# Kernel tuning notes

Hardware: AMD Instinct MI355X
Metric: run time of the kernel (lower is better)

Reference implementation:

```python
import jax, jax.numpy as jnp
import numpy as np

B, T, S_ENC, D, H, E, K = 4, 1024, 64, 1024, 16, 8, 2
DK = D // H
HID = 4 * D
NEG = -65504.0
EPS = 1e-5


def rmsnorm(x, w):
    return w * (x * jax.lax.rsqrt(jnp.mean(x * x, axis=-1, keepdims=True) + EPS))


def mha(xq, xk, xv, mask, wq, wk, wv, wo):
    # linear (no bias): y = x @ W.T
    q = jnp.einsum('bsd,ed->bse', xq, wq).reshape(xq.shape[0], -1, H, DK).transpose(0, 2, 1, 3)
    k = jnp.einsum('bsd,ed->bse', xk, wk).reshape(xk.shape[0], -1, H, DK).transpose(0, 2, 1, 3)
    v = jnp.einsum('bsd,ed->bse', xv, wv).reshape(xv.shape[0], -1, H, DK).transpose(0, 2, 1, 3)
    scores = jnp.einsum('bhqd,bhkd->bhqk', q, k) / jnp.sqrt(jnp.float32(DK))
    scores = jnp.where(mask[:, None, :, :] == 0, NEG, scores)
    attn = jax.nn.softmax(scores, axis=-1)
    out = jnp.einsum('bhqk,bhkd->bhqd', attn, v)
    out = out.transpose(0, 2, 1, 3).reshape(xq.shape[0], -1, D)
    return jnp.einsum('bsd,ed->bse', out, wo)


def moe_ffn(x, gate_w, exp_w1, exp_w2, sh_w1, sh_w2):
    b, s, d = x.shape
    xf = x.reshape(-1, d)                                     # [N, D]
    # shared expert
    sh = jnp.einsum('nd,hd->nh', xf, sh_w1)
    sh = jax.nn.silu(sh)
    sh = jnp.einsum('nh,dh->nd', sh, sh_w2)
    # gating
    logits = jnp.einsum('nd,ed->ne', xf, gate_w)              # [N, E]
    topk_vals, topk_idx = jax.lax.top_k(logits, K)
    topk_gates = jax.nn.softmax(topk_vals, axis=-1)
    n = xf.shape[0]
    gates = jnp.zeros((n, E), dtype=xf.dtype).at[jnp.arange(n)[:, None], topk_idx].set(topk_gates)
    # all experts computed densely (as in the torch code), then gated
    h = jnp.einsum('nd,ehd->neh', xf, exp_w1)                 # [N, E, 4D]
    h = jax.nn.silu(h)
    eo = jnp.einsum('neh,edh->ned', h, exp_w2)                # [N, E, D]
    sel = jnp.einsum('ned,ne->nd', eo, gates)
    return (sh + sel).reshape(b, s, d)


def setup_inputs() -> dict:
    key = jax.random.key(0)
    ks = jax.random.split(key, 16)
    sd = 1.0 / np.sqrt(D)
    inp = {
        'x': jax.random.normal(ks[0], (B, T, D), jnp.float32),
        'encoder_output': jax.random.normal(ks[1], (B, S_ENC, D), jnp.float32),
        'tgt_mask': jnp.tril(jnp.ones((T, T), jnp.int32))[None].repeat(B, 0),
        'src_mask': jnp.ones((B, T, S_ENC), jnp.int32),
        'norm1_w': jnp.ones((D,), jnp.float32),
        'norm2_w': jnp.ones((D,), jnp.float32),
        'norm3_w': jnp.ones((D,), jnp.float32),
        'sa_wq': jax.random.normal(ks[2], (D, D), jnp.float32) * sd,
        'sa_wk': jax.random.normal(ks[3], (D, D), jnp.float32) * sd,
        'sa_wv': jax.random.normal(ks[4], (D, D), jnp.float32) * sd,
        'sa_wo': jax.random.normal(ks[5], (D, D), jnp.float32) * sd,
        'ca_wq': jax.random.normal(ks[6], (D, D), jnp.float32) * sd,
        'ca_wk': jax.random.normal(ks[7], (D, D), jnp.float32) * sd,
        'ca_wv': jax.random.normal(ks[8], (D, D), jnp.float32) * sd,
        'ca_wo': jax.random.normal(ks[9], (D, D), jnp.float32) * sd,
        'gate_w': jax.random.normal(ks[10], (E, D), jnp.float32) * 0.02,
        'exp_w1': jax.random.normal(ks[11], (E, HID, D), jnp.float32) * sd,
        'exp_w2': jax.random.normal(ks[12], (E, D, HID), jnp.float32) / np.sqrt(HID),
        'sh_w1': jax.random.normal(ks[13], (HID, D), jnp.float32) * sd,
        'sh_w2': jax.random.normal(ks[14], (D, HID), jnp.float32) / np.sqrt(HID),
    }
    return inp


def reference(x, encoder_output, tgt_mask, src_mask, norm1_w, norm2_w, norm3_w,
              sa_wq, sa_wk, sa_wv, sa_wo, ca_wq, ca_wk, ca_wv, ca_wo,
              gate_w, exp_w1, exp_w2, sh_w1, sh_w2):
    xn = rmsnorm(x, norm1_w)
    h = x + mha(xn, xn, xn, tgt_mask, sa_wq, sa_wk, sa_wv, sa_wo)
    hn = rmsnorm(h, norm2_w)
    h = h + mha(hn, encoder_output, encoder_output, src_mask, ca_wq, ca_wk, ca_wv, ca_wo)
    hn = rmsnorm(h, norm3_w)
    return h + moe_ffn(hn, gate_w, exp_w1, exp_w2, sh_w1, sh_w2)
```

## Files before the change

kernel.cpp:

```cpp
#include <hip/hip_runtime.h>
#include <hip/hip_bf16.h>
#include <cstdint>
#include <cstddef>
#include <math.h>

typedef __attribute__((ext_vector_type(8))) short bf16x8;
typedef __attribute__((ext_vector_type(4))) float f32x4;
typedef __attribute__((ext_vector_type(4))) short s16x4;

static __device__ __forceinline__ short f2bf(float f) {
  union { __hip_bfloat16 b; short s; } u;
  u.b = __float2bfloat16(f);
  return u.s;
}

static __device__ __forceinline__ float bf2f(short s) {
  union { unsigned u; float f; } v;
  v.u = ((unsigned)(unsigned short)s) << 16;
  return v.f;
}

static __device__ __forceinline__ void gload_lds16(const short* g, short* l) {
  __builtin_amdgcn_global_load_lds((const __attribute__((address_space(1))) void*)g,
                                   (__attribute__((address_space(3))) void*)l,
                                   16, 0, 0);
}

__global__ __launch_bounds__(256) void cvt_k(const float* __restrict__ src,
                                             short* __restrict__ dst, long n4) {
  long i = (long)blockIdx.x * blockDim.x + threadIdx.x;
  long stride = (long)gridDim.x * blockDim.x;
  for (; i < n4; i += stride) {
    float4 v = ((const float4*)src)[i];
    s16x4 o;
    o.x = f2bf(v.x); o.y = f2bf(v.y); o.z = f2bf(v.z); o.w = f2bf(v.w);
    ((s16x4*)dst)[i] = o;
  }
}

__global__ __launch_bounds__(256) void cvt2_k(const float* __restrict__ src,
                                              short* __restrict__ hi,
                                              short* __restrict__ lo, long n4) {
  long i = (long)blockIdx.x * blockDim.x + threadIdx.x;
  long stride = (long)gridDim.x * blockDim.x;
  for (; i < n4; i += stride) {
    float4 v = ((const float4*)src)[i];
    s16x4 h, l;
    h.x = f2bf(v.x); l.x = f2bf(v.x - bf2f(h.x));
    h.y = f2bf(v.y); l.y = f2bf(v.y - bf2f(h.y));
    h.z = f2bf(v.z); l.z = f2bf(v.z - bf2f(h.z));
    h.w = f2bf(v.w); l.w = f2bf(v.w - bf2f(h.w));
    ((s16x4*)hi)[i] = h;
    ((s16x4*)lo)[i] = l;
  }
}

__global__ __launch_bounds__(256) void rms2_k(const float* __restrict__ x,
                                              const float* __restrict__ w,
                                              short* __restrict__ hi,
                                              short* __restrict__ lo) {
  const int row = blockIdx.x, tid = threadIdx.x;
  const float* xr = x + (size_t)row * 1024;
  float4 v = *(const float4*)&xr[tid * 4];
  float ss = v.x * v.x + v.y * v.y + v.z * v.z + v.w * v.w;
#pragma unroll
  for (int off = 32; off; off >>= 1) ss += __shfl_down(ss, off);
  __shared__ float red[4];
  if ((tid & 63) == 0) red[tid >> 6] = ss;
  __syncthreads();
  float rs = rsqrtf((red[0] + red[1] + red[2] + red[3]) * (1.f / 1024.f) + 1e-5f);
  float4 wv = *(const float4*)&w[tid * 4];
  float o0 = v.x * rs * wv.x, o1 = v.y * rs * wv.y;
  float o2 = v.z * rs * wv.z, o3 = v.w * rs * wv.w;
  s16x4 h, l;
  h.x = f2bf(o0); l.x = f2bf(o0 - bf2f(h.x));
  h.y = f2bf(o1); l.y = f2bf(o1 - bf2f(h.y));
  h.z = f2bf(o2); l.z = f2bf(o2 - bf2f(h.z));
  h.w = f2bf(o3); l.w = f2bf(o3 - bf2f(h.w));
  const size_t ib = (size_t)row * 1024 + tid * 4;
  *(s16x4*)&hi[ib] = h;
  *(s16x4*)&lo[ib] = l;
}

__global__ __launch_bounds__(256) void rms_k(const float* __restrict__ x,
                                             const float* __restrict__ w,
                                             short* __restrict__ obf) {
  const int row = blockIdx.x, tid = threadIdx.x;
  const float* xr = x + (size_t)row * 1024;
  float4 v = *(const float4*)&xr[tid * 4];
  float ss = v.x * v.x + v.y * v.y + v.z * v.z + v.w * v.w;
#pragma unroll
  for (int off = 32; off; off >>= 1) ss += __shfl_down(ss, off);
  __shared__ float red[4];
  if ((tid & 63) == 0) red[tid >> 6] = ss;
  __syncthreads();
  float rs = rsqrtf((red[0] + red[1] + red[2] + red[3]) * (1.f / 1024.f) + 1e-5f);
  float4 wv = *(const float4*)&w[tid * 4];
  s16x4 ob;
  ob.x = f2bf(v.x * rs * wv.x); ob.y = f2bf(v.y * rs * wv.y);
  ob.z = f2bf(v.z * rs * wv.z); ob.w = f2bf(v.w * rs * wv.w);
  *(s16x4*)&obf[(size_t)row * 1024 + tid * 4] = ob;
}

template <int EPI>
__global__ __launch_bounds__(256)
void gemm3_k(const short* __restrict__ Ah, const short* __restrict__ Al,
             const short* __restrict__ Bh, const short* __restrict__ Bl,
             float* __restrict__ C, const float* __restrict__ resid,
             short* __restrict__ Ch, short* __restrict__ Cl,
             int M, int N, int K) {
  __shared__ short sAh[128 * 32];
  __shared__ short sAl[128 * 32];
  __shared__ short sBh[128 * 32];
  __shared__ short sBl[128 * 32];

  const int bn = blockIdx.x, bm = blockIdx.y;
  const int tid = threadIdx.x;
  const int lane = tid & 63, wv = tid >> 6;
  const int rch = lane >> 2;
  const int cch = (((lane & 3) ^ (rch & 3)) << 3);
  const int wr = wv >> 1, wc = wv & 1;
  const int lr = lane & 15, lg = lane >> 4;
  const int c0 = wv * 2, c1 = wv * 2 + 1;
  const int sw = ((lg ^ (lr & 3)) << 3);

  const int ra0 = bm * 128 + c0 * 16 + rch;
  const int ra1 = bm * 128 + c1 * 16 + rch;
  const int rb0 = bn * 128 + c0 * 16 + rch, rb1 = bn * 128 + c1 * 16 + rch;

  f32x4 acc[4][4];
#pragma unroll
  for (int m = 0; m < 4; m++)
#pragma unroll
    for (int n = 0; n < 4; n++) acc[m][n] = (f32x4){0.f, 0.f, 0.f, 0.f};

  const int nk = K >> 5;
  for (int kt = 0; kt < nk; ++kt) {
    __syncthreads();
    const int colk = (kt << 5) + cch;
    gload_lds16(Ah + (size_t)ra0 * K + colk, &sAh[c0 * 512]);
    gload_lds16(Ah + (size_t)ra1 * K + colk, &sAh[c1 * 512]);
    gload_lds16(Al + (size_t)ra0 * K + colk, &sAl[c0 * 512]);
    gload_lds16(Al + (size_t)ra1 * K + colk, &sAl[c1 * 512]);
    gload_lds16(Bh + (size_t)rb0 * K + colk, &sBh[c0 * 512]);
    gload_lds16(Bh + (size_t)rb1 * K + colk, &sBh[c1 * 512]);
    gload_lds16(Bl + (size_t)rb0 * K + colk, &sBl[c0 * 512]);
    gload_lds16(Bl + (size_t)rb1 * K + colk, &sBl[c1 * 512]);
    __syncthreads();
    bf16x8 ah[4], al[4], bh[4], bl[4];
#pragma unroll
    for (int m = 0; m < 4; m++) {
      const int o = (wr * 64 + m * 16 + lr) * 32 + sw;
      ah[m] = *(const bf16x8*)&sAh[o];
      al[m] = *(const bf16x8*)&sAl[o];
    }
#pragma unroll
    for (int n = 0; n < 4; n++) {
      const int o = (wc * 64 + n * 16 + lr) * 32 + sw;
      bh[n] = *(const bf16x8*)&sBh[o];
      bl[n] = *(const bf16x8*)&sBl[o];
    }
#pragma unroll
    for (int m = 0; m < 4; m++)
#pragma unroll
      for (int n = 0; n < 4; n++) {
        acc[m][n] = __builtin_amdgcn_mfma_f32_16x16x32_bf16(ah[m], bh[n], acc[m][n], 0, 0, 0);
        acc[m][n] = __builtin_amdgcn_mfma_f32_16x16x32_bf16(al[m], bh[n], acc[m][n], 0, 0, 0);
        acc[m][n] = __builtin_amdgcn_mfma_f32_16x16x32_bf16(ah[m], bl[n], acc[m][n], 0, 0, 0);
      }
  }

  const int cbase = bn * 128 + wc * 64;
#pragma unroll
  for (int m = 0; m < 4; m++) {
    const int rl = bm * 128 + wr * 64 + m * 16 + lg * 4;
#pragma unroll
    for (int n = 0; n < 4; n++) {
      f32x4 v = acc[m][n];
      const int col = cbase + n * 16 + lr;
#pragma unroll
      for (int j = 0; j < 4; j++) {
        const size_t idx = (size_t)(rl + j) * N + col;
        if (EPI == 0) {
          C[idx] = v[j];
        } else if (EPI == 2) {
          C[idx] = v[j] + resid[idx];
        } else {
          short hh = f2bf(v[j]);
          Ch[idx] = hh;
          Cl[idx] = f2bf(v[j] - bf2f(hh));
        }
      }
    }
  }
}

template <bool CAUSAL>
__global__ __launch_bounds__(256)
void attn3_k(const short* __restrict__ Qh, const short* __restrict__ Ql, int ldq,
             const short* __restrict__ Kh, const short* __restrict__ Kl, int ldk,
             const short* __restrict__ Vh, const short* __restrict__ Vl, int ldv,
             short* __restrict__ Oh, short* __restrict__ Ol, int ldo,
             int Tq, int Tkv, float scale) {
  __shared__ short sKh[64 * 72], sKl[64 * 72];
  __shared__ short sVh[64 * 72], sVl[64 * 72];
  __shared__ short sPh[4][16 * 72], sPl[4][16 * 72];

  const int idx = blockIdx.x;
  const int qb = 15 - (idx >> 6);
  const int h = (idx >> 2) & 15;
  const int b = idx & 3;
  const int tid = threadIdx.x, lane = tid & 63, wv = tid >> 6;
  const int hoff = h * 64;
  const int lr = lane & 15, lg = lane >> 4;
  const int qlo = wv * 16;

  bf16x8 qhf[2], qlf[2];
  {
    const size_t qrow = (size_t)(b * Tq + qb * 64 + qlo + lr) * ldq + hoff;
#pragma unroll
    for (int ks = 0; ks < 2; ks++) {
      qhf[ks] = *(const bf16x8*)&Qh[qrow + ks * 32 + lg * 8];
      qlf[ks] = *(const bf16x8*)&Ql[qrow + ks * 32 + lg * 8];
    }
  }

  float m_run = -1e30f, l_run = 0.f;
  f32x4 o[4];
#pragma unroll
  for (int n = 0; n < 4; n++) o[n] = (f32x4){0.f, 0.f, 0.f, 0.f};

  const int ntiles = CAUSAL ? (qb + 1) : (Tkv >> 6);
  for (int kt = 0; kt < ntiles; ++kt) {
    __syncthreads();
#pragma unroll
    for (int j = 0; j < 2; j++) {
      int c = j * 256 + tid;
      int row = c >> 3, col = (c & 7) << 3;
      size_t gk = (size_t)(b * Tkv + kt * 64 + row) * ldk + hoff + col;
      *(bf16x8*)&sKh[row * 72 + col] = *(const bf16x8*)&Kh[gk];
      *(bf16x8*)&sKl[row * 72 + col] = *(const bf16x8*)&Kl[gk];
      size_t gv = (size_t)(b * Tkv + kt * 64 + row) * ldv + hoff + col;
      bf16x8 vh = *(const bf16x8*)&Vh[gv];
      bf16x8 vl = *(const bf16x8*)&Vl[gv];
#pragma unroll
      for (int i = 0; i < 8; i++) {
        sVh[(col + i) * 72 + row] = vh[i];
        sVl[(col + i) * 72 + row] = vl[i];
      }
    }
    __syncthreads();

    f32x4 st[4];
#pragma unroll
    for (int jk = 0; jk < 4; jk++) st[jk] = (f32x4){0.f, 0.f, 0.f, 0.f};
#pragma unroll
    for (int ks = 0; ks < 2; ks++) {
#pragma unroll
      for (int jk = 0; jk < 4; jk++) {
        const int o2 = (jk * 16 + lr) * 72 + ks * 32 + lg * 8;
        bf16x8 kh = *(const bf16x8*)&sKh[o2];
        bf16x8 kl = *(const bf16x8*)&sKl[o2];
        st[jk] = __builtin_amdgcn_mfma_f32_16x16x32_bf16(kh, qhf[ks], st[jk], 0, 0, 0);
        st[jk] = __builtin_amdgcn_mfma_f32_16x16x32_bf16(kl, qhf[ks], st[jk], 0, 0, 0);
        st[jk] = __builtin_amdgcn_mfma_f32_16x16x32_bf16(kh, qlf[ks], st[jk], 0, 0, 0);
      }
    }

    const int qg = qb * 64 + qlo + lr;
    float s[16];
    float tmax = -1e30f;
#pragma unroll
    for (int jk = 0; jk < 4; jk++)
#pragma unroll
      for (int r2 = 0; r2 < 4; r2++) {
        float xv = st[jk][r2] * scale;
        if (CAUSAL && kt == qb) {
          int kvidx = kt * 64 + jk * 16 + lg * 4 + r2;
          if (kvidx > qg) xv = -1e30f;
        }
        s[jk * 4 + r2] = xv;
        tmax = fmaxf(tmax, xv);
      }
    tmax = fmaxf(tmax, __shfl_xor(tmax, 16));
    tmax = fmaxf(tmax, __shfl_xor(tmax, 32));
    float m_new = fmaxf(m_run, tmax);
    float alpha = __expf(m_run - m_new);
    float tsum = 0.f;
#pragma unroll
    for (int i = 0; i < 16; i++) {
      float ev = (s[i] <= -1e29f) ? 0.f : __expf(s[i] - m_new);
      s[i] = ev;
      tsum += ev;
    }
    tsum += __shfl_xor(tsum, 16);
    tsum += __shfl_xor(tsum, 32);
    l_run = l_run * alpha + tsum;
    m_run = m_new;

    short* pwh = &sPh[wv][0];
    short* pwl = &sPl[wv][0];
#pragma unroll
    for (int jk = 0; jk < 4; jk++) {
      s16x4 ph, pl;
      float e0 = s[jk * 4 + 0], e1 = s[jk * 4 + 1], e2 = s[jk * 4 + 2], e3 = s[jk * 4 + 3];
      ph.x = f2bf(e0); pl.x = f2bf(e0 - bf2f(ph.x));
      ph.y = f2bf(e1); pl.y = f2bf(e1 - bf2f(ph.y));
      ph.z = f2bf(e2); pl.z = f2bf(e2 - bf2f(ph.z));
      ph.w = f2bf(e3); pl.w = f2bf(e3 - bf2f(ph.w));
      *(s16x4*)&pwh[lr * 72 + jk * 16 + lg * 4] = ph;
      *(s16x4*)&pwl[lr * 72 + jk * 16 + lg * 4] = pl;
    }
#pragma unroll
    for (int r2 = 0; r2 < 4; r2++) {
      float al = __shfl(alpha, lg * 4 + r2);
#pragma unroll
      for (int db = 0; db < 4; db++) o[db][r2] *= al;
    }
    __syncthreads();

#pragma unroll
    for (int ks = 0; ks < 2; ks++) {
      bf16x8 pah = *(const bf16x8*)&pwh[lr * 72 + ks * 32 + lg * 8];
      bf16x8 pal = *(const bf16x8*)&pwl[lr * 72 + ks * 32 + lg * 8];
#pragma unroll
      for (int db = 0; db < 4; db++) {
        const int o2 = (db * 16 + lr) * 72 + ks * 32 + lg * 8;
        bf16x8 vfh = *(const bf16x8*)&sVh[o2];
        bf16x8 vfl = *(const bf16x8*)&sVl[o2];
        o[db] = __builtin_amdgcn_mfma_f32_16x16x32_bf16(pah, vfh, o[db], 0, 0, 0);
        o[db] = __builtin_amdgcn_mfma_f32_16x16x32_bf16(pal, vfh, o[db], 0, 0, 0);
        o[db] = __builtin_amdgcn_mfma_f32_16x16x32_bf16(pah, vfl, o[db], 0, 0, 0);
      }
    }
  }

  float rinv = 1.f / l_run;
#pragma unroll
  for (int r2 = 0; r2 < 4; r2++) {
    float inv = __shfl(rinv, lg * 4 + r2);
    int token = b * Tq + qb * 64 + qlo + lg * 4 + r2;
#pragma unroll
    for (int db = 0; db < 4; db++) {
      float vv = o[db][r2] * inv;
      short hh = f2bf(vv);
      const size_t ob = (size_t)token * ldo + hoff + db * 16 + lr;
      Oh[ob] = hh;
      Ol[ob] = f2bf(vv - bf2f(hh));
    }
  }
}

template <int EPI, int MODE>
__global__ __launch_bounds__(512)
void gemm_bt_k(const short* __restrict__ A, const short* __restrict__ B,
               void* C, int M, int N, int K,
               const int* __restrict__ row_map,
               const int* __restrict__ counts,
               const int* __restrict__ offs) {
  __shared__ short sA[128 * 64];
  __shared__ short sB[128 * 64];
  __shared__ int sRow[128];

  const int tid = threadIdx.x;
  const int bn = blockIdx.x, bm = blockIdx.y;
  const int e = blockIdx.z;
  const int cnt = counts[e];
  const int base = offs[e];
  if (bm * 128 >= cnt) return;
  const short* Bp = B + (size_t)e * N * K;

  const int lane = tid & 63, wid = tid >> 6;
  const int wr = wid >> 2, wc = wid & 3;
  const int lr = lane & 15, lg = lane >> 4;
  const int lrow = lane >> 3;
  const int lcc = ((lane & 7) ^ lrow) << 3;

  if (MODE == 1) {
    if (tid < 128) {
      int r = bm * 128 + tid;
      sRow[tid] = (r < cnt) ? row_map[base + r] : row_map[base];
    }
    __syncthreads();
  }
  int rag[2], rbg[2];
#pragma unroll
  for (int i = 0; i < 2; i++) {
    const int rl = wid * 8 + i * 64 + lrow;
    if (MODE == 2) {
      rag[i] = base + ((bm * 128 + rl < cnt) ? (bm * 128 + rl) : 0);
    } else {
      rag[i] = sRow[rl];
    }
    rbg[i] = bn * 128 + rl;
  }

  f32x4 acc[4][2];
#pragma unroll
  for (int m = 0; m < 4; m++)
#pragma unroll
    for (int n = 0; n < 2; n++) acc[m][n] = (f32x4){0.f, 0.f, 0.f, 0.f};

  const int nk = K >> 6;
  for (int kt = 0; kt < nk; ++kt) {
    __syncthreads();
    const int colk = (kt << 6) + lcc;
#pragma unroll
    for (int i = 0; i < 2; i++) {
      gload_lds16(A + (size_t)rag[i] * K + colk, &sA[(wid * 8 + i * 64) * 64]);
      gload_lds16(Bp + (size_t)rbg[i] * K + colk, &sB[(wid * 8 + i * 64) * 64]);
    }
    __syncthreads();
#pragma unroll
    for (int ks = 0; ks < 2; ks++) {
      const int sw = ((((ks << 2) + lg) ^ (lr & 7)) << 3);
      bf16x8 a[4], b[2];
#pragma unroll
      for (int m = 0; m < 4; m++)
        a[m] = *(const bf16x8*)&sA[(wr * 64 + m * 16 + lr) * 64 + sw];
#pragma unroll
      for (int n = 0; n < 2; n++)
        b[n] = *(const bf16x8*)&sB[(wc * 32 + n * 16 + lr) * 64 + sw];
#pragma unroll
      for (int m = 0; m < 4; m++)
#pragma unroll
        for (int n = 0; n < 2; n++)
          acc[m][n] = __builtin_amdgcn_mfma_f32_16x16x32_bf16(a[m], b[n], acc[m][n], 0, 0, 0);
    }
  }

#pragma unroll
  for (int m = 0; m < 4; m++) {
    const int rl = wr * 64 + m * 16 + lg * 4;
#pragma unroll
    for (int n = 0; n < 2; n++) {
      f32x4 v = acc[m][n];
      const int col = bn * 128 + wc * 32 + n * 16 + lr;
#pragma unroll
      for (int j = 0; j < 4; j++) {
        const int rloc = bm * 128 + rl + j;
        if (rloc >= cnt) continue;
        const size_t idx = (size_t)(base + rloc) * N + col;
        float xv = v[j];
        if (EPI == 1) {
          float s = xv / (1.f + __expf(-xv));
          ((short*)C)[idx] = f2bf(s);
        } else {
          ((short*)C)[idx] = f2bf(xv);
        }
      }
    }
  }
}

__global__ __launch_bounds__(256) void gate_k(const float* __restrict__ H,
                                              const float* __restrict__ w3,
                                              const float* __restrict__ gw,
                                              int* counts, int* tok_e, int* tok_s,
                                              float* tok_g) {
  const int token = blockIdx.x * 4 + (threadIdx.x >> 6);
  const int lane = threadIdx.x & 63;
  const float* xr = H + (size_t)token * 1024;
  double a[8] = {0, 0, 0, 0, 0, 0, 0, 0};
  double ss = 0.0;
#pragma unroll
  for (int i = 0; i < 4; i++) {
    float4 xv = *(const float4*)&xr[i * 256 + lane * 4];
    float4 w3v = *(const float4*)&w3[i * 256 + lane * 4];
    ss += (double)xv.x * xv.x + (double)xv.y * xv.y + (double)xv.z * xv.z + (double)xv.w * xv.w;
    double xw0 = (double)xv.x * (double)w3v.x, xw1 = (double)xv.y * (double)w3v.y;
    double xw2 = (double)xv.z * (double)w3v.z, xw3 = (double)xv.w * (double)w3v.w;
#pragma unroll
    for (int e = 0; e < 8; e++) {
      float4 wv = *(const float4*)&gw[e * 1024 + i * 256 + lane * 4];
      a[e] += xw0 * wv.x + xw1 * wv.y + xw2 * wv.z + xw3 * wv.w;
    }
  }
#pragma unroll
  for (int off = 32; off; off >>= 1) {
    ss += __shfl_down(ss, off);
#pragma unroll
    for (int e = 0; e < 8; e++) a[e] += __shfl_down(a[e], off);
  }
  if (lane == 0) {
    double v0 = a[0]; int i0 = 0;
#pragma unroll
    for (int e = 1; e < 8; e++) if (a[e] > v0) { v0 = a[e]; i0 = e; }
    double v1 = -1e300; int i1 = 0;
#pragma unroll
    for (int e = 0; e < 8; e++) if (e != i0 && a[e] > v1) { v1 = a[e]; i1 = e; }
    double rs = 1.0 / sqrt(ss * (1.0 / 1024.0) + 1e-5);
    double t = exp((v1 - v0) * rs);
    double g0 = 1.0 / (1.0 + t);
    int s0 = atomicAdd(&counts[i0], 1);
    int s1 = atomicAdd(&counts[i1], 1);
    tok_e[2 * token] = i0; tok_e[2 * token + 1] = i1;
    tok_s[2 * token] = s0; tok_s[2 * token + 1] = s1;
    tok_g[2 * token] = (float)g0; tok_g[2 * token + 1] = (float)(1.0 - g0);
  }
}

__global__ void offsets_k(int* counts, int* offs) {
  if (threadIdx.x == 0 && blockIdx.x == 0) {
    counts[8] = 4096;
    int s = 0;
    for (int e = 0; e < 9; e++) { offs[e] = s; s += counts[e]; }
  }
}

__global__ __launch_bounds__(256) void build_rows_k(const int* __restrict__ offs,
                                                    const int* __restrict__ tok_e,
                                                    const int* __restrict__ tok_s,
                                                    int* __restrict__ row_map,
                                                    int* __restrict__ tok_row) {
  int n = blockIdx.x * 256 + threadIdx.x;
  int e0 = tok_e[2 * n], e1 = tok_e[2 * n + 1];
  int r0 = offs[e0] + tok_s[2 * n], r1 = offs[e1] + tok_s[2 * n + 1];
  row_map[r0] = n; row_map[r1] = n;
  row_map[8192 + n] = n;
  tok_row[2 * n] = r0; tok_row[2 * n + 1] = r1;
}

__global__ __launch_bounds__(256) void combine_k(const float* __restrict__ H,
                                                 const short* __restrict__ eo,
                                                 const int* __restrict__ tok_row,
                                                 const float* __restrict__ tok_g,
                                                 float* __restrict__ out) {
  const int n = blockIdx.x, t = threadIdx.x;
  const int r0 = tok_row[2 * n], r1 = tok_row[2 * n + 1];
  const float g0 = tok_g[2 * n], g1 = tok_g[2 * n + 1];
  const size_t ib = (size_t)n * 1024 + t * 4;
  float4 hv = *(const float4*)&H[ib];
  s16x4 sv = *(const s16x4*)&eo[(size_t)(8192 + n) * 1024 + t * 4];
  s16x4 a0 = *(const s16x4*)&eo[(size_t)r0 * 1024 + t * 4];
  s16x4 a1 = *(const s16x4*)&eo[(size_t)r1 * 1024 + t * 4];
  float4 ov;
  ov.x = hv.x + bf2f(sv.x) + g0 * bf2f(a0.x) + g1 * bf2f(a1.x);
  ov.y = hv.y + bf2f(sv.y) + g0 * bf2f(a0.y) + g1 * bf2f(a1.y);
  ov.z = hv.z + bf2f(sv.z) + g0 * bf2f(a0.z) + g1 * bf2f(a1.z);
  ov.w = hv.w + bf2f(sv.w) + g0 * bf2f(a0.w) + g1 * bf2f(a1.w);
  *(float4*)&out[ib] = ov;
}

extern "C" void kernel_launch(void* const* d_in, const int* in_sizes, int n_in,
                              void* d_out, int out_size, void* d_ws, size_t ws_size,
                              hipStream_t stream) {
  (void)in_sizes; (void)n_in; (void)out_size;
  const float* x     = (const float*)d_in[0];
  const float* enc   = (const float*)d_in[1];
  const float* n1w   = (const float*)d_in[4];
  const float* n2w   = (const float*)d_in[5];
  const float* n3w   = (const float*)d_in[6];
  const float* sa_wq = (const float*)d_in[7];
  const float* sa_wk = (const float*)d_in[8];
  const float* sa_wv = (const float*)d_in[9];
  const float* sa_wo = (const float*)d_in[10];
  const float* ca_wq = (const float*)d_in[11];
  const float* ca_wk = (const float*)d_in[12];
  const float* ca_wv = (const float*)d_in[13];
  const float* ca_wo = (const float*)d_in[14];
  const float* gw    = (const float*)d_in[15];
  const float* e_w1  = (const float*)d_in[16];
  const float* e_w2  = (const float*)d_in[17];
  const float* s_w1  = (const float*)d_in[18];
  const float* s_w2  = (const float*)d_in[19];
  float* out = (float*)d_out;

  char* p = (char*)d_ws;
  size_t off = 0;
  auto alloc = [&](size_t bytes) -> void* {
    void* r = p + off;
    off += (bytes + 255) & ~(size_t)255;
    return r;
  };
  short* w_all1 = (short*)alloc(9LL * 4096 * 1024 * 2);
  short* w_all2 = (short*)alloc(9LL * 1024 * 4096 * 2);
  short* xn     = (short*)alloc(4096LL * 1024 * 2);
  char*  U      = (char*)alloc(12288LL * 4096 * 2);
  short* hbuf   = (short*)U;
  float* Hb     = (float*)alloc(4096LL * 1024 * 4);
  short* eo     = (short*)alloc(12288LL * 1024 * 2);
  short* xh     = (short*)alloc(4096LL * 1024 * 2);
  short* xl     = (short*)alloc(4096LL * 1024 * 2);
  short* ench   = (short*)alloc(256LL * 1024 * 2);
  short* encl   = (short*)alloc(256LL * 1024 * 2);
  short* wsh    = (short*)alloc(3072LL * 1024 * 2);
  short* wsl    = (short*)alloc(3072LL * 1024 * 2);
  int*   counts = (int*)alloc(9 * 4);
  int*   offs   = (int*)alloc(9 * 4);
  int*   tok_e  = (int*)alloc(4096LL * 2 * 4);
  int*   tok_s  = (int*)alloc(4096LL * 2 * 4);
  float* tok_g  = (float*)alloc(4096LL * 2 * 4);
  int*   tok_row= (int*)alloc(4096LL * 2 * 4);
  int*   row_map= (int*)alloc(12288LL * 4);
  if (off > ws_size) return;

  short* qkvh = (short*)U;
  short* qkvl = qkvh + 4096LL * 3072;
  short* crossQh = (short*)U;
  short* crossQl = crossQh + 4096LL * 1024;
  short* encKVh  = crossQl + 4096LL * 1024;
  short* encKVl  = encKVh + 256LL * 2048;

  auto cvt = [&](const float* s, short* d, long n) {
    long n4 = n / 4;
    long g = (n4 + 255) / 256;
    int grid = (int)(g > 4096 ? 4096 : g);
    cvt_k<<<grid, 256, 0, stream>>>(s, d, n4);
  };
  auto cvt2 = [&](const float* s, short* h, short* l, long n) {
    long n4 = n / 4;
    long g = (n4 + 255) / 256;
    int grid = (int)(g > 4096 ? 4096 : g);
    cvt2_k<<<grid, 256, 0, stream>>>(s, h, l, n4);
  };

  cvt(e_w1, w_all1, 8L * 4096 * 1024);
  cvt(s_w1, w_all1 + 8L * 4096 * 1024, 4096L * 1024);
  cvt(e_w2, w_all2, 8L * 1024 * 4096);
  cvt(s_w2, w_all2 + 8L * 1024 * 4096, 1024L * 4096);
  cvt2(enc, ench, encl, 256L * 1024);

  rms2_k<<<4096, 256, 0, stream>>>(x, n1w, xh, xl);
  cvt2(sa_wq, wsh, wsl, 1024L * 1024);
  cvt2(sa_wk, wsh + 1048576, wsl + 1048576, 1024L * 1024);
  cvt2(sa_wv, wsh + 2097152, wsl + 2097152, 1024L * 1024);
  gemm3_k<3><<<dim3(24, 32), 256, 0, stream>>>(xh, xl, wsh, wsl, nullptr, nullptr,
      qkvh, qkvl, 4096, 3072, 1024);
  attn3_k<true><<<1024, 256, 0, stream>>>(qkvh, qkvl, 3072,
      qkvh + 1024, qkvl + 1024, 3072, qkvh + 2048, qkvl + 2048, 3072,
      xh, xl, 1024, 1024, 1024, 0.125f);
  cvt2(sa_wo, wsh, wsl, 1024L * 1024);
  gemm3_k<2><<<dim3(8, 32), 256, 0, stream>>>(xh, xl, wsh, wsl, Hb, x,
      nullptr, nullptr, 4096, 1024, 1024);

  rms2_k<<<4096, 256, 0, stream>>>(Hb, n2w, xh, xl);
  cvt2(ca_wq, wsh, wsl, 1024L * 1024);
  gemm3_k<3><<<dim3(8, 32), 256, 0, stream>>>(xh, xl, wsh, wsl, nullptr, nullptr,
      crossQh, crossQl, 4096, 1024, 1024);
  cvt2(ca_wk, wsh, wsl, 1024L * 1024);
  cvt2(ca_wv, wsh + 1048576, wsl + 1048576, 1024L * 1024);
  gemm3_k<3><<<dim3(16, 2), 256, 0, stream>>>(ench, encl, wsh, wsl, nullptr, nullptr,
      encKVh, encKVl, 256, 2048, 1024);
  attn3_k<false><<<1024, 256, 0, stream>>>(crossQh, crossQl, 1024,
      encKVh, encKVl, 2048, encKVh + 1024, encKVl + 1024, 2048,
      xh, xl, 1024, 1024, 64, 0.125f);
  cvt2(ca_wo, wsh, wsl, 1024L * 1024);
  gemm3_k<2><<<dim3(8, 32), 256, 0, stream>>>(xh, xl, wsh, wsl, Hb, Hb,
      nullptr, nullptr, 4096, 1024, 1024);

  rms_k<<<4096, 256, 0, stream>>>(Hb, n3w, xn);
  hipMemsetAsync(counts, 0, 8 * sizeof(int), stream);
  gate_k<<<1024, 256, 0, stream>>>(Hb, n3w, gw, counts, tok_e, tok_s, tok_g);
  offsets_k<<<1, 1, 0, stream>>>(counts, offs);
  build_rows_k<<<16, 256, 0, stream>>>(offs, tok_e, tok_s, row_map, tok_row);
  gemm_bt_k<1, 1><<<dim3(32, 32, 9), 512, 0, stream>>>(xn, w_all1, hbuf,
      4096, 4096, 1024, row_map, counts, offs);
  gemm_bt_k<3, 2><<<dim3(8, 32, 9), 512, 0, stream>>>(hbuf, w_all2, eo,
      4096, 1024, 4096, row_map, counts, offs);

  combine_k<<<4096, 256, 0, stream>>>(Hb, eo, tok_row, tok_g, out);
}
```

Before: 951.1 us.

## Batch split-bf16 weight conversions, fuse final RMSNorm into gating, widen gemm3 to 512 threads

All eight attention weight matrices and the encoder output are now split into hi/lo bf16 by a single multi-source conversion launch into a dedicated buffer, replacing nine separate small launches. The separate final RMSNorm kernel is removed and its bf16 output is written by the gating kernel, which already loads each row and computes its sum of squares. The split-precision gemm3 kernel moves from 4 to 8 waves per 128x128 tile, each wave computing a 64x32 sub-tile, which lowers accumulator registers per wave and raises wave count. The trade-offs are a larger weight workspace and more LDS fragment loads per block.

```diff
diff --git a/kernel.cpp b/kernel.cpp
--- a/kernel.cpp
+++ b/kernel.cpp
@@ -38,21 +38,31 @@
   }
 }
 
-__global__ __launch_bounds__(256) void cvt2_k(const float* __restrict__ src,
-                                              short* __restrict__ hi,
-                                              short* __restrict__ lo, long n4) {
-  long i = (long)blockIdx.x * blockDim.x + threadIdx.x;
-  long stride = (long)gridDim.x * blockDim.x;
-  for (; i < n4; i += stride) {
-    float4 v = ((const float4*)src)[i];
-    s16x4 h, l;
-    h.x = f2bf(v.x); l.x = f2bf(v.x - bf2f(h.x));
-    h.y = f2bf(v.y); l.y = f2bf(v.y - bf2f(h.y));
-    h.z = f2bf(v.z); l.z = f2bf(v.z - bf2f(h.z));
-    h.w = f2bf(v.w); l.w = f2bf(v.w - bf2f(h.w));
-    ((s16x4*)hi)[i] = h;
-    ((s16x4*)lo)[i] = l;
-  }
+__global__ __launch_bounds__(256) void cvt2multi_k(
+    const float* s0, const float* s1, const float* s2, const float* s3,
+    const float* s4, const float* s5, const float* s6, const float* s7,
+    const float* s8, short* __restrict__ hi, short* __restrict__ lo) {
+  const int y = blockIdx.y;
+  const long n4 = (y < 8) ? 262144 : 65536;
+  long i = (long)blockIdx.x * 256 + threadIdx.x;
+  if (i >= n4) return;
+  const float* src;
+  switch (y) {
+    case 0: src = s0; break; case 1: src = s1; break;
+    case 2: src = s2; break; case 3: src = s3; break;
+    case 4: src = s4; break; case 5: src = s5; break;
+    case 6: src = s6; break; case 7: src = s7; break;
+    default: src = s8; break;
+  }
+  float4 v = ((const float4*)src)[i];
+  s16x4 h, l;
+  h.x = f2bf(v.x); l.x = f2bf(v.x - bf2f(h.x));
+  h.y = f2bf(v.y); l.y = f2bf(v.y - bf2f(h.y));
+  h.z = f2bf(v.z); l.z = f2bf(v.z - bf2f(h.z));
+  h.w = f2bf(v.w); l.w = f2bf(v.w - bf2f(h.w));
+  const long o = (long)y * 262144 + i;
+  ((s16x4*)hi)[o] = h;
+  ((s16x4*)lo)[o] = l;
 }
 
 __global__ __launch_bounds__(256) void rms2_k(const float* __restrict__ x,
@@ -82,28 +92,8 @@
   *(s16x4*)&lo[ib] = l;
 }
 
-__global__ __launch_bounds__(256) void rms_k(const float* __restrict__ x,
-                                             const float* __restrict__ w,
-                                             short* __restrict__ obf) {
-  const int row = blockIdx.x, tid = threadIdx.x;
-  const float* xr = x + (size_t)row * 1024;
-  float4 v = *(const float4*)&xr[tid * 4];
-  float ss = v.x * v.x + v.y * v.y + v.z * v.z + v.w * v.w;
-#pragma unroll
-  for (int off = 32; off; off >>= 1) ss += __shfl_down(ss, off);
-  __shared__ float red[4];
-  if ((tid & 63) == 0) red[tid >> 6] = ss;
-  __syncthreads();
-  float rs = rsqrtf((red[0] + red[1] + red[2] + red[3]) * (1.f / 1024.f) + 1e-5f);
-  float4 wv = *(const float4*)&w[tid * 4];
-  s16x4 ob;
-  ob.x = f2bf(v.x * rs * wv.x); ob.y = f2bf(v.y * rs * wv.y);
-  ob.z = f2bf(v.z * rs * wv.z); ob.w = f2bf(v.w * rs * wv.w);
-  *(s16x4*)&obf[(size_t)row * 1024 + tid * 4] = ob;
-}
-
 template <int EPI>
-__global__ __launch_bounds__(256)
+__global__ __launch_bounds__(512)
 void gemm3_k(const short* __restrict__ Ah, const short* __restrict__ Al,
              const short* __restrict__ Bh, const short* __restrict__ Bl,
              float* __restrict__ C, const float* __restrict__ resid,
@@ -116,38 +106,32 @@
 
   const int bn = blockIdx.x, bm = blockIdx.y;
   const int tid = threadIdx.x;
-  const int lane = tid & 63, wv = tid >> 6;
+  const int lane = tid & 63, wid = tid >> 6;
+  const int wr = wid >> 2, wc = wid & 3;
+  const int lr = lane & 15, lg = lane >> 4;
   const int rch = lane >> 2;
   const int cch = (((lane & 3) ^ (rch & 3)) << 3);
-  const int wr = wv >> 1, wc = wv & 1;
-  const int lr = lane & 15, lg = lane >> 4;
-  const int c0 = wv * 2, c1 = wv * 2 + 1;
   const int sw = ((lg ^ (lr & 3)) << 3);
 
-  const int ra0 = bm * 128 + c0 * 16 + rch;
-  const int ra1 = bm * 128 + c1 * 16 + rch;
-  const int rb0 = bn * 128 + c0 * 16 + rch, rb1 = bn * 128 + c1 * 16 + rch;
-
-  f32x4 acc[4][4];
+  const int ra = bm * 128 + wid * 16 + rch;
+  const int rb = bn * 128 + wid * 16 + rch;
+
+  f32x4 acc[4][2];
 #pragma unroll
   for (int m = 0; m < 4; m++)
 #pragma unroll
-    for (int n = 0; n < 4; n++) acc[m][n] = (f32x4){0.f, 0.f, 0.f, 0.f};
+    for (int n = 0; n < 2; n++) acc[m][n] = (f32x4){0.f, 0.f, 0.f, 0.f};
 
   const int nk = K >> 5;
   for (int kt = 0; kt < nk; ++kt) {
     __syncthreads();
     const int colk = (kt << 5) + cch;
-    gload_lds16(Ah + (size_t)ra0 * K + colk, &sAh[c0 * 512]);
-    gload_lds16(Ah + (size_t)ra1 * K + colk, &sAh[c1 * 512]);
-    gload_lds16(Al + (size_t)ra0 * K + colk, &sAl[c0 * 512]);
-    gload_lds16(Al + (size_t)ra1 * K + colk, &sAl[c1 * 512]);
-    gload_lds16(Bh + (size_t)rb0 * K + colk, &sBh[c0 * 512]);
-    gload_lds16(Bh + (size_t)rb1 * K + colk, &sBh[c1 * 512]);
-    gload_lds16(Bl + (size_t)rb0 * K + colk, &sBl[c0 * 512]);
-    gload_lds16(Bl + (size_t)rb1 * K + colk, &sBl[c1 * 512]);
-    __syncthreads();
-    bf16x8 ah[4], al[4], bh[4], bl[4];
+    gload_lds16(Ah + (size_t)ra * K + colk, &sAh[wid * 512]);
+    gload_lds16(Al + (size_t)ra * K + colk, &sAl[wid * 512]);
+    gload_lds16(Bh + (size_t)rb * K + colk, &sBh[wid * 512]);
+    gload_lds16(Bl + (size_t)rb * K + colk, &sBl[wid * 512]);
+    __syncthreads();
+    bf16x8 ah[4], al[4], bh[2], bl[2];
 #pragma unroll
     for (int m = 0; m < 4; m++) {
       const int o = (wr * 64 + m * 16 + lr) * 32 + sw;
@@ -155,29 +139,28 @@
       al[m] = *(const bf16x8*)&sAl[o];
     }
 #pragma unroll
-    for (int n = 0; n < 4; n++) {
-      const int o = (wc * 64 + n * 16 + lr) * 32 + sw;
+    for (int n = 0; n < 2; n++) {
+      const int o = (wc * 32 + n * 16 + lr) * 32 + sw;
       bh[n] = *(const bf16x8*)&sBh[o];
       bl[n] = *(const bf16x8*)&sBl[o];
     }
 #pragma unroll
     for (int m = 0; m < 4; m++)
 #pragma unroll
-      for (int n = 0; n < 4; n++) {
+      for (int n = 0; n < 2; n++) {
         acc[m][n] = __builtin_amdgcn_mfma_f32_16x16x32_bf16(ah[m], bh[n], acc[m][n], 0, 0, 0);
         acc[m][n] = __builtin_amdgcn_mfma_f32_16x16x32_bf16(al[m], bh[n], acc[m][n], 0, 0, 0);
         acc[m][n] = __builtin_amdgcn_mfma_f32_16x16x32_bf16(ah[m], bl[n], acc[m][n], 0, 0, 0);
       }
   }
 
-  const int cbase = bn * 128 + wc * 64;
 #pragma unroll
   for (int m = 0; m < 4; m++) {
     const int rl = bm * 128 + wr * 64 + m * 16 + lg * 4;
 #pragma unroll
-    for (int n = 0; n < 4; n++) {
+    for (int n = 0; n < 2; n++) {
       f32x4 v = acc[m][n];
-      const int col = cbase + n * 16 + lr;
+      const int col = bn * 128 + wc * 32 + n * 16 + lr;
 #pragma unroll
       for (int j = 0; j < 4; j++) {
         const size_t idx = (size_t)(rl + j) * N + col;
@@ -456,17 +439,20 @@
 __global__ __launch_bounds__(256) void gate_k(const float* __restrict__ H,
                                               const float* __restrict__ w3,
                                               const float* __restrict__ gw,
+                                              short* __restrict__ xn,
                                               int* counts, int* tok_e, int* tok_s,
                                               float* tok_g) {
   const int token = blockIdx.x * 4 + (threadIdx.x >> 6);
   const int lane = threadIdx.x & 63;
   const float* xr = H + (size_t)token * 1024;
+  float4 xv4[4], w34[4];
   double a[8] = {0, 0, 0, 0, 0, 0, 0, 0};
   double ss = 0.0;
 #pragma unroll
   for (int i = 0; i < 4; i++) {
-    float4 xv = *(const float4*)&xr[i * 256 + lane * 4];
-    float4 w3v = *(const float4*)&w3[i * 256 + lane * 4];
+    xv4[i] = *(const float4*)&xr[i * 256 + lane * 4];
+    w34[i] = *(const float4*)&w3[i * 256 + lane * 4];
+    float4 xv = xv4[i], w3v = w34[i];
     ss += (double)xv.x * xv.x + (double)xv.y * xv.y + (double)xv.z * xv.z + (double)xv.w * xv.w;
     double xw0 = (double)xv.x * (double)w3v.x, xw1 = (double)xv.y * (double)w3v.y;
     double xw2 = (double)xv.z * (double)w3v.z, xw3 = (double)xv.w * (double)w3v.w;
@@ -477,10 +463,22 @@
     }
   }
 #pragma unroll
+  for (int off = 32; off; off >>= 1) ss += __shfl_xor(ss, off);
+#pragma unroll
   for (int off = 32; off; off >>= 1) {
-    ss += __shfl_down(ss, off);
 #pragma unroll
     for (int e = 0; e < 8; e++) a[e] += __shfl_down(a[e], off);
+  }
+  const double rs_d = 1.0 / sqrt(ss * (1.0 / 1024.0) + 1e-5);
+  const float rs = (float)rs_d;
+#pragma unroll
+  for (int i = 0; i < 4; i++) {
+    s16x4 ob;
+    ob.x = f2bf(xv4[i].x * rs * w34[i].x);
+    ob.y = f2bf(xv4[i].y * rs * w34[i].y);
+    ob.z = f2bf(xv4[i].z * rs * w34[i].z);
+    ob.w = f2bf(xv4[i].w * rs * w34[i].w);
+    *(s16x4*)&xn[(size_t)token * 1024 + i * 256 + lane * 4] = ob;
   }
   if (lane == 0) {
     double v0 = a[0]; int i0 = 0;
@@ -489,8 +487,7 @@
     double v1 = -1e300; int i1 = 0;
 #pragma unroll
     for (int e = 0; e < 8; e++) if (e != i0 && a[e] > v1) { v1 = a[e]; i1 = e; }
-    double rs = 1.0 / sqrt(ss * (1.0 / 1024.0) + 1e-5);
-    double t = exp((v1 - v0) * rs);
+    double t = exp((v1 - v0) * rs_d);
     double g0 = 1.0 / (1.0 + t);
     int s0 = atomicAdd(&counts[i0], 1);
     int s1 = atomicAdd(&counts[i1], 1);
@@ -582,10 +579,8 @@
   short* eo     = (short*)alloc(12288LL * 1024 * 2);
   short* xh     = (short*)alloc(4096LL * 1024 * 2);
   short* xl     = (short*)alloc(4096LL * 1024 * 2);
-  short* ench   = (short*)alloc(256LL * 1024 * 2);
-  short* encl   = (short*)alloc(256LL * 1024 * 2);
-  short* wsh    = (short*)alloc(3072LL * 1024 * 2);
-  short* wsl    = (short*)alloc(3072LL * 1024 * 2);
+  short* wsplH  = (short*)alloc(8650752LL * 2);
+  short* wsplL  = (short*)alloc(8650752LL * 2);
   int*   counts = (int*)alloc(9 * 4);
   int*   offs   = (int*)alloc(9 * 4);
   int*   tok_e  = (int*)alloc(4096LL * 2 * 4);
@@ -595,6 +590,19 @@
   int*   row_map= (int*)alloc(12288LL * 4);
   if (off > ws_size) return;
 
+  short* wQKVh = wsplH;
+  short* wQKVl = wsplL;
+  short* wOh   = wsplH + 3145728;
+  short* wOl   = wsplL + 3145728;
+  short* wCQh  = wsplH + 4194304;
+  short* wCQl  = wsplL + 4194304;
+  short* wCKVh = wsplH + 5242880;
+  short* wCKVl = wsplL + 5242880;
+  short* wCOh  = wsplH + 7340032;
+  short* wCOl  = wsplL + 7340032;
+  short* ench  = wsplH + 8388608;
+  short* encl  = wsplL + 8388608;
+
   short* qkvh = (short*)U;
   short* qkvl = qkvh + 4096LL * 3072;
   short* crossQh = (short*)U;
@@ -608,50 +616,37 @@
     int grid = (int)(g > 4096 ? 4096 : g);
     cvt_k<<<grid, 256, 0, stream>>>(s, d, n4);
   };
-  auto cvt2 = [&](const float* s, short* h, short* l, long n) {
-    long n4 = n / 4;
-    long g = (n4 + 255) / 256;
-    int grid = (int)(g > 4096 ? 4096 : g);
-    cvt2_k<<<grid, 256, 0, stream>>>(s, h, l, n4);
-  };
+
+  cvt2multi_k<<<dim3(1024, 9), 256, 0, stream>>>(sa_wq, sa_wk, sa_wv, sa_wo,
+      ca_wq, ca_wk, ca_wv, ca_wo, enc, wsplH, wsplL);
 
   cvt(e_w1, w_all1, 8L * 4096 * 1024);
   cvt(s_w1, w_all1 + 8L * 4096 * 1024, 4096L * 1024);
   cvt(e_w2, w_all2, 8L * 1024 * 4096);
   cvt(s_w2, w_all2 + 8L * 1024 * 4096, 1024L * 4096);
-  cvt2(enc, ench, encl, 256L * 1024);
 
   rms2_k<<<4096, 256, 0, stream>>>(x, n1w, xh, xl);
-  cvt2(sa_wq, wsh, wsl, 1024L * 1024);
-  cvt2(sa_wk, wsh + 1048576, wsl + 1048576, 1024L * 1024);
-  cvt2(sa_wv, wsh + 2097152, wsl + 2097152, 1024L * 1024);
-  gemm3_k<3><<<dim3(24, 32), 256, 0, stream>>>(xh, xl, wsh, wsl, nullptr, nullptr,
+  gemm3_k<3><<<dim3(24, 32), 512, 0, stream>>>(xh, xl, wQKVh, wQKVl, nullptr, nullptr,
       qkvh, qkvl, 4096, 3072, 1024);
   attn3_k<true><<<1024, 256, 0, stream>>>(qkvh, qkvl, 3072,
       qkvh + 1024, qkvl + 1024, 3072, qkvh + 2048, qkvl + 2048, 3072,
       xh, xl, 1024, 1024, 1024, 0.125f);
-  cvt2(sa_wo, wsh, wsl, 1024L * 1024);
-  gemm3_k<2><<<dim3(8, 32), 256, 0, stream>>>(xh, xl, wsh, wsl, Hb, x,
+  gemm3_k<2><<<dim3(8, 32), 512, 0, stream>>>(xh, xl, wOh, wOl, Hb, x,
       nullptr, nullptr, 4096, 1024, 1024);
 
   rms2_k<<<4096, 256, 0, stream>>>(Hb, n2w, xh, xl);
-  cvt2(ca_wq, wsh, wsl, 1024L * 1024);
-  gemm3_k<3><<<dim3(8, 32), 256, 0, stream>>>(xh, xl, wsh, wsl, nullptr, nullptr,
+  gemm3_k<3><<<dim3(8, 32), 512, 0, stream>>>(xh, xl, wCQh, wCQl, nullptr, nullptr,
       crossQh, crossQl, 4096, 1024, 1024);
-  cvt2(ca_wk, wsh, wsl, 1024L * 1024);
-  cvt2(ca_wv, wsh + 1048576, wsl + 1048576, 1024L * 1024);
-  gemm3_k<3><<<dim3(16, 2), 256, 0, stream>>>(ench, encl, wsh, wsl, nullptr, nullptr,
+  gemm3_k<3><<<dim3(16, 2), 512, 0, stream>>>(ench, encl, wCKVh, wCKVl, nullptr, nullptr,
       encKVh, encKVl, 256, 2048, 1024);
   attn3_k<false><<<1024, 256, 0, stream>>>(crossQh, crossQl, 1024,
       encKVh, encKVl, 2048, encKVh + 1024, encKVl + 1024, 2048,
       xh, xl, 1024, 1024, 64, 0.125f);
-  cvt2(ca_wo, wsh, wsl, 1024L * 1024);
-  gemm3_k<2><<<dim3(8, 32), 256, 0, stream>>>(xh, xl, wsh, wsl, Hb, Hb,
+  gemm3_k<2><<<dim3(8, 32), 512, 0, stream>>>(xh, xl, wCOh, wCOl, Hb, Hb,
       nullptr, nullptr, 4096, 1024, 1024);
 
-  rms_k<<<4096, 256, 0, stream>>>(Hb, n3w, xn);
   hipMemsetAsync(counts, 0, 8 * sizeof(int), stream);
-  gate_k<<<1024, 256, 0, stream>>>(Hb, n3w, gw, counts, tok_e, tok_s, tok_g);
+  gate_k<<<1024, 256, 0, stream>>>(Hb, n3w, gw, xn, counts, tok_e, tok_s, tok_g);
   offsets_k<<<1, 1, 0, stream>>>(counts, offs);
   build_rows_k<<<16, 256, 0, stream>>>(offs, tok_e, tok_s, row_map, tok_row);
   gemm_bt_k<1, 1><<<dim3(32, 32, 9), 512, 0, stream>>>(xn, w_all1, hbuf,
```

Measured after the change: 936.4 us (median of 2 runs). No clear change (-1.5%).
